# Performance work log

Hardware: AMD Instinct MI355X
Metric: run time of the kernel (lower is better)

The kernel has to match this reference:

```python
import jax, jax.numpy as jnp
import numpy as np

N_NODES = 4096
N_EDGES = 65536
BS = 16
LEAKY_SLOPE = 0.01
BN_EPS = 1e-5


def _init(key, shape, scale=0.02):
    return (jax.random.normal(key, shape, dtype=jnp.float32) * scale)


def setup_inputs() -> dict:
    key = jax.random.key(0)
    ks = jax.random.split(key, 20)
    x_in = jax.random.normal(ks[0], (N_NODES, 8500), dtype=jnp.float32)
    edge_index = jax.random.randint(ks[1], (2, N_EDGES), 0, N_NODES, dtype=jnp.int64)
    return {
        "x_in": x_in,
        "edge_index": edge_index,
        # SAGEConv params: Wl (neighbor lin, with bias), Wr (root lin, no bias)
        "W1l": _init(ks[2], (320, 8500)), "b1": jnp.zeros((320,), jnp.float32), "W1r": _init(ks[3], (320, 8500)),
        "W2l": _init(ks[4], (180, 320)),  "b2": jnp.zeros((180,), jnp.float32), "W2r": _init(ks[5], (180, 320)),
        "W3l": _init(ks[6], (90, 180)),   "b3": jnp.zeros((90,), jnp.float32),  "W3r": _init(ks[7], (90, 180)),
        "W4l": _init(ks[8], (50, 90)),    "b4": jnp.zeros((50,), jnp.float32),  "W4r": _init(ks[9], (50, 90)),
        "Wf1": _init(ks[10], (32, 50)),   "bf1": jnp.zeros((32,), jnp.float32),
        "Wf2": _init(ks[11], (16, 32)),   "bf2": jnp.zeros((16,), jnp.float32),
        "Wf3": _init(ks[12], (1, 16)),    "bf3": jnp.zeros((1,), jnp.float32),
    }


def _sage(x, src, dst, Wl, bl, Wr):
    # PyG SAGEConv: out = lin_l(mean_{j in N(i)} x_j) + lin_r(x_i)
    agg = jax.ops.segment_sum(x[src], dst, num_segments=N_NODES)          # [N, F]
    deg = jax.ops.segment_sum(jnp.ones_like(dst, dtype=x.dtype), dst, num_segments=N_NODES)
    mean = agg / jnp.maximum(deg, 1.0)[:, None]
    return mean @ Wl.T + bl + x @ Wr.T


def _leaky(x):
    return jnp.where(x >= 0, x, LEAKY_SLOPE * x)


def _bn(x):
    # F.batch_norm(x, None, None, training=True): per-feature, biased var, no affine
    m = jnp.mean(x, axis=0)
    v = jnp.mean((x - m) ** 2, axis=0)
    return (x - m) / jnp.sqrt(v + BN_EPS)


def reference(x_in, edge_index,
              W1l, b1, W1r, W2l, b2, W2r, W3l, b3, W3r, W4l, b4, W4r,
              Wf1, bf1, Wf2, bf2, Wf3, bf3):
    src, dst = edge_index[0], edge_index[1]
    x = _bn(_leaky(_sage(x_in, src, dst, W1l, b1, W1r)))
    x = _bn(_leaky(_sage(x, src, dst, W2l, b2, W2r)))
    x = _bn(_leaky(_sage(x, src, dst, W3l, b3, W3r)))
    x = _bn(_leaky(_sage(x, src, dst, W4l, b4, W4r)))
    # get_batch: label i -> floor(i / (N/BS)); global_add_pool == segment sum
    x = x.reshape(BS, N_NODES // BS, -1).sum(axis=1)                      # [BS, 50]
    x = x @ Wf1.T + bf1
    x = x @ Wf2.T + bf2
    x = x @ Wf3.T + bf3
    return x
```

## Files before the change

kernel.cpp:

```cpp
#include <hip/hip_runtime.h>
#include <stdint.h>

#define NN 4096
#define NE 65536
#define LEAKY 0.01f
#define BN_EPS 1e-5f

typedef float f32x4 __attribute__((ext_vector_type(4)));
typedef __bf16 bf16x8 __attribute__((ext_vector_type(8)));
typedef unsigned short u16x8 __attribute__((ext_vector_type(8)));

static __device__ __forceinline__ unsigned short f2bf(float v) {
  unsigned int u = __float_as_uint(v);
  u += 0x7fff + ((u >> 16) & 1);
  return (unsigned short)(u >> 16);
}

typedef __attribute__((address_space(1))) void gvoid;
typedef __attribute__((address_space(3))) void lvoid;

static __device__ __forceinline__ void async16(const void* g, void* l) {
  __builtin_amdgcn_global_load_lds((gvoid*)(uintptr_t)g,
                                   (lvoid*)(uint32_t)(uintptr_t)l, 16, 0, 0);
}


static __device__ __forceinline__ void pack_w_seg(int lblk, const float* __restrict__ Wl,
                                                  const float* __restrict__ Wr,
                                                  unsigned short* __restrict__ dst,
                                                  int Fout, int Fin, int Kp, int Np) {
  int nb = Kp >> 3;
  int idx = lblk * 256 + threadIdx.x;
  if (idx >= Np * nb) return;
  int row = idx / nb, kb = idx - row * nb;
  int g = kb >> 3, b = kb & 7;
  int dkb = (g << 3) | ((b + row) & 7);
  const float* src = nullptr;
  if (row < Fout)          src = Wl + (size_t)row * Fin;
  else if (row < 2 * Fout) src = Wr + (size_t)(row - Fout) * Fin;
  u16x8 st;
#pragma unroll
  for (int o = 0; o < 8; ++o) {
    int k = kb * 8 + o;
    float v = (src && k < Fin) ? src[k] : 0.f;
    st[o] = f2bf(v);
  }
  *(u16x8*)&dst[(size_t)row * Kp + dkb * 8] = st;
}

#define PX_BLK   17024
#define PW1_BLK   2660
#define PW2_BLK     60
#define PW3_BLK     24
#define PW4_BLK      8
#define CD_BLK     256
#define SETUP_BLK (PX_BLK + PW1_BLK + PW2_BLK + PW3_BLK + PW4_BLK + CD_BLK)

__global__ __launch_bounds__(256) void setup_all(
    const float* __restrict__ x, const int* __restrict__ dsti,
    const float* __restrict__ W1l, const float* __restrict__ W1r,
    const float* __restrict__ W2l, const float* __restrict__ W2r,
    const float* __restrict__ W3l, const float* __restrict__ W3r,
    const float* __restrict__ W4l, const float* __restrict__ W4r,
    unsigned short* __restrict__ xbf, unsigned short* __restrict__ wb1,
    unsigned short* __restrict__ wb2, unsigned short* __restrict__ wb3,
    unsigned short* __restrict__ wb4, int* __restrict__ deg) {
  int blk = blockIdx.x;
  if (blk < PX_BLK) {
    int idx = blk * 256 + threadIdx.x;
    int row = idx / 1064, kb = idx - row * 1064;
    int g = kb >> 3, b = kb & 7;
    int dkb = (g << 3) | ((b + row) & 7);
    const float* src = x + (size_t)row * 8500 + kb * 8;
    float v[8];
    if (kb < 1062) {
      f32x4 a = *(const f32x4*)src;
      f32x4 c = *(const f32x4*)(src + 4);
#pragma unroll
      for (int o = 0; o < 4; ++o) { v[o] = a[o]; v[o + 4] = c[o]; }
    } else {
#pragma unroll
      for (int o = 0; o < 8; ++o) {
        int k = kb * 8 + o;
        v[o] = (k < 8500) ? x[(size_t)row * 8500 + k] : 0.f;
      }
    }
    u16x8 st;
#pragma unroll
    for (int o = 0; o < 8; ++o) st[o] = f2bf(v[o]);
    *(u16x8*)&xbf[(size_t)row * 8512 + dkb * 8] = st;
  } else if (blk < PX_BLK + PW1_BLK) {
    pack_w_seg(blk - PX_BLK, W1l, W1r, wb1, 320, 8500, 8512, 640);
  } else if (blk < PX_BLK + PW1_BLK + PW2_BLK) {
    pack_w_seg(blk - PX_BLK - PW1_BLK, W2l, W2r, wb2, 180, 320, 320, 384);
  } else if (blk < PX_BLK + PW1_BLK + PW2_BLK + PW3_BLK) {
    pack_w_seg(blk - PX_BLK - PW1_BLK - PW2_BLK, W3l, W3r, wb3, 90, 180, 192, 256);
  } else if (blk < PX_BLK + PW1_BLK + PW2_BLK + PW3_BLK + PW4_BLK) {
    pack_w_seg(blk - PX_BLK - PW1_BLK - PW2_BLK - PW3_BLK, W4l, W4r, wb4, 50, 90, 128, 128);
  } else {
    int e = (blk - (SETUP_BLK - CD_BLK)) * 256 + threadIdx.x;
    atomicAdd(&deg[dsti[e]], 1);
  }
}


__global__ __launch_bounds__(1024) void scan_deg(const int* __restrict__ deg,
                                                 int* __restrict__ off) {
  __shared__ int s[NN];
  int t = threadIdx.x;
  for (int i = t; i < NN; i += 1024) s[i] = deg[i];
  __syncthreads();
  for (int step = 1; step < NN; step <<= 1) {
    int v[4];
#pragma unroll
    for (int j = 0; j < 4; ++j) {
      int i = t + j * 1024;
      v[j] = (i >= step) ? s[i - step] : 0;
    }
    __syncthreads();
#pragma unroll
    for (int j = 0; j < 4; ++j) s[t + j * 1024] += v[j];
    __syncthreads();
  }
  for (int i = t; i < NN; i += 1024) off[i] = (i == 0) ? 0 : s[i - 1];
}

__global__ void scatter_edges(const int* __restrict__ src_idx,
                              const int* __restrict__ dst_idx,
                              const int* __restrict__ off, int* __restrict__ cursor,
                              int* __restrict__ eix) {
  int e = blockIdx.x * 256 + threadIdx.x;
  if (e < NE) {
    int d = dst_idx[e];
    int pos = atomicAdd(&cursor[d], 1);
    eix[off[d] + pos] = src_idx[e];
  }
}

__global__ __launch_bounds__(256) void gemm_bt(const unsigned short* __restrict__ A,
                                               const unsigned short* __restrict__ B,
                                               float* __restrict__ C, int N, int K,
                                               int M) {
  __shared__ unsigned short smem[2 * 128 * 64];
  unsigned short* As = smem;
  unsigned short* Bs = smem + 128 * 64;

  const int t = threadIdx.x;
  const int bm = blockIdx.x, bn = blockIdx.y;
  const int lane = t & 63;
  const int wave = t >> 6;
  const int wm = (wave & 1) * 64, wn = (wave >> 1) * 64;
  const int l16 = lane & 15, quad = lane >> 4;

  const int ksteps = K >> 6;
  const int gz = (int)gridDim.z;
  const int per = (ksteps + gz - 1) / gz;
  const int k0 = (int)blockIdx.z * per;
  int k1 = k0 + per; if (k1 > ksteps) k1 = ksteps;

  f32x4 zero = {0.f, 0.f, 0.f, 0.f};
  f32x4 acc[4][4];
#pragma unroll
  for (int i = 0; i < 4; ++i)
#pragma unroll
    for (int j = 0; j < 4; ++j) acc[i][j] = zero;

  const int srow = t >> 3;
  const int scol = (t & 7) * 8;
  const unsigned short* Abase = A + (size_t)(bm * 128) * K + scol;
  const unsigned short* Bbase = B + (size_t)(bn * 128) * K + scol;

  for (int kt = k0; kt < k1; ++kt) {
    const unsigned short* Ag = Abase + kt * 64;
    const unsigned short* Bg = Bbase + kt * 64;
#pragma unroll
    for (int p = 0; p < 4; ++p) {
      int row = p * 32 + srow;
      async16(Ag + (size_t)row * K, &As[row * 64 + scol]);
    }
#pragma unroll
    for (int p = 0; p < 4; ++p) {
      int row = p * 32 + srow;
      async16(Bg + (size_t)row * K, &Bs[row * 64 + scol]);
    }
    __syncthreads();
#pragma unroll
    for (int kh = 0; kh < 2; ++kh) {
      const int s8 = ((kh * 4 + quad + l16) & 7) * 8;
      bf16x8 af[4], bfr[4];
#pragma unroll
      for (int i = 0; i < 4; ++i)
        af[i] = *(const bf16x8*)&As[(wm + i * 16 + l16) * 64 + s8];
#pragma unroll
      for (int j = 0; j < 4; ++j)
        bfr[j] = *(const bf16x8*)&Bs[(wn + j * 16 + l16) * 64 + s8];
#pragma unroll
      for (int i = 0; i < 4; ++i)
#pragma unroll
        for (int j = 0; j < 4; ++j)
          acc[i][j] = __builtin_amdgcn_mfma_f32_16x16x32_bf16(af[i], bfr[j], acc[i][j], 0, 0, 0);
    }
    __syncthreads();
  }

  float* Cb = C + (size_t)blockIdx.z * M * N;
#pragma unroll
  for (int i = 0; i < 4; ++i) {
    int rbase = bm * 128 + wm + i * 16 + quad * 4;
#pragma unroll
    for (int j = 0; j < 4; ++j) {
      int col = bn * 128 + wn + j * 16 + l16;
      float* cp = Cb + (size_t)rbase * N + col;
#pragma unroll
      for (int r = 0; r < 4; ++r) cp[(size_t)r * N] = acc[i][j][r];
    }
  }
}

__global__ void reduce4(float* __restrict__ y) {
  int idx = blockIdx.x * 256 + threadIdx.x;
  f32x4* p = (f32x4*)y;
  const int S = NN * 640 / 4;
  f32x4 v = p[idx];
  v += p[idx + S];
  v += p[idx + 2 * S];
  v += p[idx + 3 * S];
  p[idx] = v;
}

__global__ __launch_bounds__(256) void sage_agg(
    const float* __restrict__ y, const int* __restrict__ off,
    const int* __restrict__ deg, const int* __restrict__ eix,
    const float* __restrict__ bias, float* __restrict__ z, int F, int ldy) {
  int i = blockIdx.x;
  int tx = threadIdx.x, ty = threadIdx.y;
  int f4 = (blockIdx.y * 64 + tx) * 4;
  __shared__ int se[64];
  __shared__ float red[3][64][4];
  int start = off[i], d = deg[i];
  bool active = (f4 < F);
  f32x4 s = {0.f, 0.f, 0.f, 0.f};
  for (int base = 0; base < d; base += 64) {
    __syncthreads();
    if (ty == 0 && base + tx < d) se[tx] = eix[start + base + tx];
    __syncthreads();
    int end = d - base; if (end > 64) end = 64;
    if (active) {
      for (int e = ty; e < end; e += 4)
        s += *(const f32x4*)&y[(size_t)se[e] * ldy + f4];
    }
  }
  if (ty > 0) *(f32x4*)red[ty - 1][tx] = s;
  __syncthreads();
  if (ty == 0 && active) {
    s += *(const f32x4*)red[0][tx];
    s += *(const f32x4*)red[1][tx];
    s += *(const f32x4*)red[2][tx];
    float inv = 1.f / (float)(d > 1 ? d : 1);
    int cnt = F - f4; if (cnt > 4) cnt = 4;
    const float* yr = &y[(size_t)i * ldy + F + f4];
    float* zo = &z[(size_t)i * F + f4];
    for (int j = 0; j < cnt; ++j) {
      float w = s[j] * inv + yr[j] + bias[f4 + j];
      zo[j] = (w >= 0.f) ? w : LEAKY * w;
    }
  }
}


__global__ __launch_bounds__(256) void bn_part(const float* __restrict__ z,
                                               float* __restrict__ sums, int F) {
  int tx = threadIdx.x, ty = threadIdx.y;
  int f = blockIdx.x * 64 + tx;
  float s = 0.f, s2 = 0.f;
  if (f < F) {
    int r0 = blockIdx.y * 512 + ty * 128;
    for (int j = 0; j < 128; ++j) {
      float v = z[(size_t)(r0 + j) * F + f];
      s += v; s2 += v * v;
    }
  }
  __shared__ float ls[4][64], ls2[4][64];
  ls[ty][tx] = s; ls2[ty][tx] = s2;
  __syncthreads();
  if (ty == 0 && f < F) {
    float S  = ls[0][tx] + ls[1][tx] + ls[2][tx] + ls[3][tx];
    float S2 = ls2[0][tx] + ls2[1][tx] + ls2[2][tx] + ls2[3][tx];
    atomicAdd(&sums[f], S);
    atomicAdd(&sums[F + f], S2);
  }
}

__global__ void bn_norm8(const float* __restrict__ z, const float* __restrict__ sums,
                         unsigned short* __restrict__ xout, int F, int Kp) {
  int nb = Kp >> 3;
  int idx = blockIdx.x * 256 + threadIdx.x;
  int row = idx / nb, kb = idx - row * nb;
  int g = kb >> 3, b = kb & 7;
  int dkb = (g << 3) | ((b + row) & 7);
  u16x8 st;
#pragma unroll
  for (int o = 0; o < 8; ++o) {
    int k = kb * 8 + o;
    float v = 0.f;
    if (k < F) {
      float m  = sums[k] * (1.f / NN);
      float var = sums[F + k] * (1.f / NN) - m * m;
      float rs = rsqrtf(var + BN_EPS);
      v = (z[(size_t)row * F + k] - m) * rs;
    }
    st[o] = f2bf(v);
  }
  *(u16x8*)&xout[(size_t)row * Kp + dkb * 8] = st;
}

__global__ void pool_fc(const float* __restrict__ z,
                        const float* __restrict__ sums,
                        const float* __restrict__ Wf1, const float* __restrict__ bf1,
                        const float* __restrict__ Wf2, const float* __restrict__ bf2,
                        const float* __restrict__ Wf3, const float* __restrict__ bf3,
                        float* __restrict__ out) {
  __shared__ float pool[50];
  __shared__ float h1[32], h2[16];
  int b = blockIdx.x, t = threadIdx.x;
  if (t < 50) {
    float s = 0.f;
    for (int r = 0; r < 256; ++r) s += z[(size_t)(b * 256 + r) * 50 + t];
    float m  = sums[t] * (1.f / NN);
    float var = sums[50 + t] * (1.f / NN) - m * m;
    float rs = rsqrtf(var + BN_EPS);
    pool[t] = (s - 256.f * m) * rs;
  }
  __syncthreads();
  if (t < 32) {
    float s = bf1[t];
    for (int f = 0; f < 50; ++f) s += pool[f] * Wf1[t * 50 + f];
    h1[t] = s;
  }
  __syncthreads();
  if (t < 16) {
    float s = bf2[t];
    for (int f = 0; f < 32; ++f) s += h1[f] * Wf2[t * 32 + f];
    h2[t] = s;
  }
  __syncthreads();
  if (t == 0) {
    float s = bf3[0];
    for (int f = 0; f < 16; ++f) s += h2[f] * Wf3[f];
    out[b] = s;
  }
}


extern "C" void kernel_launch(void* const* d_in, const int* in_sizes, int n_in,
                              void* d_out, int out_size, void* d_ws, size_t ws_size,
                              hipStream_t stream) {
  const float* x_in = (const float*)d_in[0];
  const int* ei = (const int*)d_in[1];
  const float* W1l = (const float*)d_in[2];
  const float* b1  = (const float*)d_in[3];
  const float* W1r = (const float*)d_in[4];
  const float* W2l = (const float*)d_in[5];
  const float* b2  = (const float*)d_in[6];
  const float* W2r = (const float*)d_in[7];
  const float* W3l = (const float*)d_in[8];
  const float* b3  = (const float*)d_in[9];
  const float* W3r = (const float*)d_in[10];
  const float* W4l = (const float*)d_in[11];
  const float* b4  = (const float*)d_in[12];
  const float* W4r = (const float*)d_in[13];
  const float* Wf1 = (const float*)d_in[14];
  const float* bf1 = (const float*)d_in[15];
  const float* Wf2 = (const float*)d_in[16];
  const float* bf2 = (const float*)d_in[17];
  const float* Wf3 = (const float*)d_in[18];
  const float* bf3 = (const float*)d_in[19];
  float* out = (float*)d_out;
  (void)in_sizes; (void)n_in; (void)out_size;

  char* ws = (char*)d_ws;
  size_t off = 0;
  auto alloc = [&](size_t bytes) -> void* {
    void* p = ws + off;
    off = (off + bytes + 255) & ~(size_t)255;
    return p;
  };
  unsigned short* xbf = (unsigned short*)alloc((size_t)NN * 8512 * 2);
  unsigned short* wb1 = (unsigned short*)alloc((size_t)640 * 8512 * 2);
  unsigned short* wb2 = (unsigned short*)alloc((size_t)384 * 320 * 2);
  unsigned short* wb3 = (unsigned short*)alloc((size_t)256 * 192 * 2);
  unsigned short* wb4 = (unsigned short*)alloc((size_t)128 * 128 * 2);
  float* y    = (float*)alloc((size_t)4 * NN * 640 * 4);
  float* z    = (float*)alloc((size_t)NN * 320 * 4);
  int* deg    = (int*)alloc(NN * 4);
  int* cursor = (int*)alloc(NN * 4);
  float* bnsum = (float*)alloc(1280 * 4);
  int* offb   = (int*)alloc(NN * 4);
  int* eix    = (int*)alloc(NE * 4);
  if (ws_size < off) return;
  float* bns1 = bnsum;
  float* bns2 = bnsum + 640;
  float* bns3 = bnsum + 1000;
  float* bns4 = bnsum + 1180;

  hipMemsetAsync(deg, 0, 2 * NN * 4 + 1280 * 4, stream);

  setup_all<<<dim3(SETUP_BLK), dim3(256), 0, stream>>>(
      x_in, ei + NE, W1l, W1r, W2l, W2r, W3l, W3r, W4l, W4r,
      xbf, wb1, wb2, wb3, wb4, deg);
  scan_deg<<<dim3(1), dim3(1024), 0, stream>>>(deg, offb);
  scatter_edges<<<dim3(NE / 256), dim3(256), 0, stream>>>(ei, ei + NE, offb, cursor, eix);

  gemm_bt<<<dim3(32, 5, 4), dim3(256), 0, stream>>>(xbf, wb1, y, 640, 8512, NN);
  reduce4<<<dim3(NN * 640 / 4 / 256), dim3(256), 0, stream>>>(y);
  sage_agg<<<dim3(NN, 2), dim3(64, 4), 0, stream>>>(y, offb, deg, eix, b1, z, 320, 640);
  bn_part<<<dim3(5, 8), dim3(64, 4), 0, stream>>>(z, bns1, 320);
  bn_norm8<<<dim3(NN * 40 / 256), dim3(256), 0, stream>>>(z, bns1, xbf, 320, 320);

  gemm_bt<<<dim3(32, 3, 1), dim3(256), 0, stream>>>(xbf, wb2, y, 384, 320, NN);
  sage_agg<<<dim3(NN, 1), dim3(64, 4), 0, stream>>>(y, offb, deg, eix, b2, z, 180, 384);
  bn_part<<<dim3(3, 8), dim3(64, 4), 0, stream>>>(z, bns2, 180);
  bn_norm8<<<dim3(NN * 24 / 256), dim3(256), 0, stream>>>(z, bns2, xbf, 180, 192);

  gemm_bt<<<dim3(32, 2, 1), dim3(256), 0, stream>>>(xbf, wb3, y, 256, 192, NN);
  sage_agg<<<dim3(NN, 1), dim3(64, 4), 0, stream>>>(y, offb, deg, eix, b3, z, 90, 256);
  bn_part<<<dim3(2, 8), dim3(64, 4), 0, stream>>>(z, bns3, 90);
  bn_norm8<<<dim3(NN * 16 / 256), dim3(256), 0, stream>>>(z, bns3, xbf, 90, 128);

  gemm_bt<<<dim3(32, 1, 1), dim3(256), 0, stream>>>(xbf, wb4, y, 128, 128, NN);
  sage_agg<<<dim3(NN, 1), dim3(64, 4), 0, stream>>>(y, offb, deg, eix, b4, z, 50, 128);
  bn_part<<<dim3(1, 8), dim3(64, 4), 0, stream>>>(z, bns4, 50);

  pool_fc<<<dim3(16), dim3(64), 0, stream>>>(z, bns4, Wf1, bf1, Wf2, bf2, Wf3, bf3, out);
}
```

Measured before the change: 516.4 us.

## Fuse post-GEMM pipeline into one persistent kernel with grid barriers

Replaces the chain of small launches (scan, scatter, split-K reduce, aggregation, BN partials, BN normalize, small GEMMs, pooling/FC) with a single 256-block persistent kernel that separates the stages with a software grid barrier. The first GEMM's split-K is raised from 4 to 8 when the workspace allows, and the slice reduction moves into the fused kernel, which runs it alongside the degree scan. The goal is to remove per-launch overhead and idle gaps between many tiny kernels. In exchange, every stage is limited to 256 blocks, there are many barrier round trips, and the barrier relies on all 256 blocks being co-resident.

```diff
diff --git a/kernel.cpp b/kernel.cpp
--- a/kernel.cpp
+++ b/kernel.cpp
@@ -103,40 +103,6 @@
   }
 }
 
-
-__global__ __launch_bounds__(1024) void scan_deg(const int* __restrict__ deg,
-                                                 int* __restrict__ off) {
-  __shared__ int s[NN];
-  int t = threadIdx.x;
-  for (int i = t; i < NN; i += 1024) s[i] = deg[i];
-  __syncthreads();
-  for (int step = 1; step < NN; step <<= 1) {
-    int v[4];
-#pragma unroll
-    for (int j = 0; j < 4; ++j) {
-      int i = t + j * 1024;
-      v[j] = (i >= step) ? s[i - step] : 0;
-    }
-    __syncthreads();
-#pragma unroll
-    for (int j = 0; j < 4; ++j) s[t + j * 1024] += v[j];
-    __syncthreads();
-  }
-  for (int i = t; i < NN; i += 1024) off[i] = (i == 0) ? 0 : s[i - 1];
-}
-
-__global__ void scatter_edges(const int* __restrict__ src_idx,
-                              const int* __restrict__ dst_idx,
-                              const int* __restrict__ off, int* __restrict__ cursor,
-                              int* __restrict__ eix) {
-  int e = blockIdx.x * 256 + threadIdx.x;
-  if (e < NE) {
-    int d = dst_idx[e];
-    int pos = atomicAdd(&cursor[d], 1);
-    eix[off[d] + pos] = src_idx[e];
-  }
-}
-
 __global__ __launch_bounds__(256) void gemm_bt(const unsigned short* __restrict__ A,
                                                const unsigned short* __restrict__ B,
                                                float* __restrict__ C, int N, int K,
@@ -217,137 +183,307 @@
   }
 }
 
-__global__ void reduce4(float* __restrict__ y) {
-  int idx = blockIdx.x * 256 + threadIdx.x;
-  f32x4* p = (f32x4*)y;
-  const int S = NN * 640 / 4;
-  f32x4 v = p[idx];
-  v += p[idx + S];
-  v += p[idx + 2 * S];
-  v += p[idx + 3 * S];
-  p[idx] = v;
-}
-
-__global__ __launch_bounds__(256) void sage_agg(
-    const float* __restrict__ y, const int* __restrict__ off,
-    const int* __restrict__ deg, const int* __restrict__ eix,
-    const float* __restrict__ bias, float* __restrict__ z, int F, int ldy) {
-  int i = blockIdx.x;
-  int tx = threadIdx.x, ty = threadIdx.y;
-  int f4 = (blockIdx.y * 64 + tx) * 4;
-  __shared__ int se[64];
-  __shared__ float red[3][64][4];
-  int start = off[i], d = deg[i];
-  bool active = (f4 < F);
-  f32x4 s = {0.f, 0.f, 0.f, 0.f};
-  for (int base = 0; base < d; base += 64) {
-    __syncthreads();
-    if (ty == 0 && base + tx < d) se[tx] = eix[start + base + tx];
-    __syncthreads();
-    int end = d - base; if (end > 64) end = 64;
-    if (active) {
-      for (int e = ty; e < end; e += 4)
-        s += *(const f32x4*)&y[(size_t)se[e] * ldy + f4];
-    }
-  }
-  if (ty > 0) *(f32x4*)red[ty - 1][tx] = s;
+
+static __device__ __forceinline__ void gbar(int* cnt, int* gen) {
   __syncthreads();
-  if (ty == 0 && active) {
-    s += *(const f32x4*)red[0][tx];
-    s += *(const f32x4*)red[1][tx];
-    s += *(const f32x4*)red[2][tx];
-    float inv = 1.f / (float)(d > 1 ? d : 1);
-    int cnt = F - f4; if (cnt > 4) cnt = 4;
-    const float* yr = &y[(size_t)i * ldy + F + f4];
-    float* zo = &z[(size_t)i * F + f4];
-    for (int j = 0; j < cnt; ++j) {
-      float w = s[j] * inv + yr[j] + bias[f4 + j];
-      zo[j] = (w >= 0.f) ? w : LEAKY * w;
-    }
-  }
-}
-
-
-__global__ __launch_bounds__(256) void bn_part(const float* __restrict__ z,
-                                               float* __restrict__ sums, int F) {
-  int tx = threadIdx.x, ty = threadIdx.y;
-  int f = blockIdx.x * 64 + tx;
-  float s = 0.f, s2 = 0.f;
-  if (f < F) {
-    int r0 = blockIdx.y * 512 + ty * 128;
-    for (int j = 0; j < 128; ++j) {
-      float v = z[(size_t)(r0 + j) * F + f];
-      s += v; s2 += v * v;
-    }
-  }
-  __shared__ float ls[4][64], ls2[4][64];
-  ls[ty][tx] = s; ls2[ty][tx] = s2;
+  if (threadIdx.x == 0) {
+    __threadfence();
+    int g = __hip_atomic_load(gen, __ATOMIC_RELAXED, __HIP_MEMORY_SCOPE_AGENT);
+    int a = __hip_atomic_fetch_add(cnt, 1, __ATOMIC_ACQ_REL, __HIP_MEMORY_SCOPE_AGENT);
+    if (a == (int)gridDim.x - 1) {
+      __hip_atomic_store(cnt, 0, __ATOMIC_RELAXED, __HIP_MEMORY_SCOPE_AGENT);
+      __hip_atomic_store(gen, g + 1, __ATOMIC_RELEASE, __HIP_MEMORY_SCOPE_AGENT);
+    } else {
+      while (__hip_atomic_load(gen, __ATOMIC_ACQUIRE, __HIP_MEMORY_SCOPE_AGENT) == g)
+        __builtin_amdgcn_s_sleep(2);
+    }
+  }
   __syncthreads();
-  if (ty == 0 && f < F) {
-    float S  = ls[0][tx] + ls[1][tx] + ls[2][tx] + ls[3][tx];
-    float S2 = ls2[0][tx] + ls2[1][tx] + ls2[2][tx] + ls2[3][tx];
-    atomicAdd(&sums[f], S);
-    atomicAdd(&sums[F + f], S2);
-  }
-}
-
-__global__ void bn_norm8(const float* __restrict__ z, const float* __restrict__ sums,
-                         unsigned short* __restrict__ xout, int F, int Kp) {
-  int nb = Kp >> 3;
-  int idx = blockIdx.x * 256 + threadIdx.x;
-  int row = idx / nb, kb = idx - row * nb;
-  int g = kb >> 3, b = kb & 7;
-  int dkb = (g << 3) | ((b + row) & 7);
-  u16x8 st;
-#pragma unroll
-  for (int o = 0; o < 8; ++o) {
-    int k = kb * 8 + o;
-    float v = 0.f;
-    if (k < F) {
-      float m  = sums[k] * (1.f / NN);
-      float var = sums[F + k] * (1.f / NN) - m * m;
-      float rs = rsqrtf(var + BN_EPS);
-      v = (z[(size_t)row * F + k] - m) * rs;
-    }
-    st[o] = f2bf(v);
-  }
-  *(u16x8*)&xout[(size_t)row * Kp + dkb * 8] = st;
-}
-
-__global__ void pool_fc(const float* __restrict__ z,
-                        const float* __restrict__ sums,
-                        const float* __restrict__ Wf1, const float* __restrict__ bf1,
-                        const float* __restrict__ Wf2, const float* __restrict__ bf2,
-                        const float* __restrict__ Wf3, const float* __restrict__ bf3,
-                        float* __restrict__ out) {
-  __shared__ float pool[50];
-  __shared__ float h1[32], h2[16];
-  int b = blockIdx.x, t = threadIdx.x;
-  if (t < 50) {
-    float s = 0.f;
-    for (int r = 0; r < 256; ++r) s += z[(size_t)(b * 256 + r) * 50 + t];
-    float m  = sums[t] * (1.f / NN);
-    float var = sums[50 + t] * (1.f / NN) - m * m;
-    float rs = rsqrtf(var + BN_EPS);
-    pool[t] = (s - 256.f * m) * rs;
-  }
-  __syncthreads();
-  if (t < 32) {
-    float s = bf1[t];
-    for (int f = 0; f < 50; ++f) s += pool[f] * Wf1[t * 50 + f];
-    h1[t] = s;
-  }
-  __syncthreads();
-  if (t < 16) {
-    float s = bf2[t];
-    for (int f = 0; f < 32; ++f) s += h1[f] * Wf2[t * 32 + f];
-    h2[t] = s;
-  }
-  __syncthreads();
-  if (t == 0) {
-    float s = bf3[0];
-    for (int f = 0; f < 16; ++f) s += h2[f] * Wf3[f];
-    out[b] = s;
+}
+
+static __device__ __forceinline__ void gemm_stage(const unsigned short* __restrict__ A,
+    const unsigned short* __restrict__ B, float* __restrict__ C, int N, int K, int nbn,
+    unsigned short* smem) {
+  unsigned short* As = smem;
+  unsigned short* Bs = smem + 128 * 64;
+  const int t = threadIdx.x;
+  const int lane = t & 63, wave = t >> 6;
+  const int wm = (wave & 1) * 64, wn = (wave >> 1) * 64;
+  const int l16 = lane & 15, quad = lane >> 4;
+  const int srow = t >> 3, scol = (t & 7) * 8;
+  const int ksteps = K >> 6;
+  const int tiles = 32 * nbn;
+  for (int u = blockIdx.x; u < tiles; u += 256) {
+    int bm = u & 31, bn = u >> 5;
+    f32x4 acc[4][4];
+#pragma unroll
+    for (int i = 0; i < 4; ++i)
+#pragma unroll
+      for (int j = 0; j < 4; ++j) acc[i][j] = (f32x4){0.f, 0.f, 0.f, 0.f};
+    const unsigned short* Abase = A + (size_t)(bm * 128) * K + scol;
+    const unsigned short* Bbase = B + (size_t)(bn * 128) * K + scol;
+    for (int kt = 0; kt < ksteps; ++kt) {
+      const unsigned short* Ag = Abase + kt * 64;
+      const unsigned short* Bg = Bbase + kt * 64;
+#pragma unroll
+      for (int p = 0; p < 4; ++p) {
+        int row = p * 32 + srow;
+        async16(Ag + (size_t)row * K, &As[row * 64 + scol]);
+      }
+#pragma unroll
+      for (int p = 0; p < 4; ++p) {
+        int row = p * 32 + srow;
+        async16(Bg + (size_t)row * K, &Bs[row * 64 + scol]);
+      }
+      __syncthreads();
+#pragma unroll
+      for (int kh = 0; kh < 2; ++kh) {
+        const int s8 = ((kh * 4 + quad + l16) & 7) * 8;
+        bf16x8 af[4], bfr[4];
+#pragma unroll
+        for (int i = 0; i < 4; ++i)
+          af[i] = *(const bf16x8*)&As[(wm + i * 16 + l16) * 64 + s8];
+#pragma unroll
+        for (int j = 0; j < 4; ++j)
+          bfr[j] = *(const bf16x8*)&Bs[(wn + j * 16 + l16) * 64 + s8];
+#pragma unroll
+        for (int i = 0; i < 4; ++i)
+#pragma unroll
+          for (int j = 0; j < 4; ++j)
+            acc[i][j] = __builtin_amdgcn_mfma_f32_16x16x32_bf16(af[i], bfr[j], acc[i][j], 0, 0, 0);
+      }
+      __syncthreads();
+    }
+#pragma unroll
+    for (int i = 0; i < 4; ++i) {
+      int rbase = bm * 128 + wm + i * 16 + quad * 4;
+#pragma unroll
+      for (int j = 0; j < 4; ++j) {
+        int col = bn * 128 + wn + j * 16 + l16;
+        float* cp = C + (size_t)rbase * N + col;
+#pragma unroll
+        for (int r = 0; r < 4; ++r) cp[(size_t)r * N] = acc[i][j][r];
+      }
+    }
+  }
+}
+
+static __device__ __forceinline__ void agg_stage(const float* __restrict__ y,
+    const int* __restrict__ off, const int* __restrict__ deg, const int* __restrict__ eix,
+    const float* __restrict__ bias, float* __restrict__ z, int F, int ldy, int nfg,
+    unsigned short* smem) {
+  const int t = threadIdx.x;
+  const int tx = t & 63, ty = t >> 6;
+  int* se = (int*)smem;
+  float* red = (float*)((char*)smem + 512);
+  const int nunits = NN * nfg;
+  for (int u = blockIdx.x; u < nunits; u += 256) {
+    int i = (nfg == 2) ? (u >> 1) : u;
+    int fg = (nfg == 2) ? (u & 1) : 0;
+    int f4 = (fg * 64 + tx) * 4;
+    int start = off[i], d = deg[i];
+    bool active = (f4 < F);
+    f32x4 s = {0.f, 0.f, 0.f, 0.f};
+    for (int base = 0; base < d; base += 64) {
+      __syncthreads();
+      if (ty == 0 && base + tx < d) se[tx] = eix[start + base + tx];
+      __syncthreads();
+      int end = d - base; if (end > 64) end = 64;
+      if (active)
+        for (int e = ty; e < end; e += 4)
+          s += *(const f32x4*)&y[(size_t)se[e] * ldy + f4];
+    }
+    if (ty > 0) *(f32x4*)&red[((ty - 1) * 64 + tx) * 4] = s;
+    __syncthreads();
+    if (ty == 0 && active) {
+      s += *(const f32x4*)&red[(tx) * 4];
+      s += *(const f32x4*)&red[(64 + tx) * 4];
+      s += *(const f32x4*)&red[(128 + tx) * 4];
+      float inv = 1.f / (float)(d > 1 ? d : 1);
+      int cnt2 = F - f4; if (cnt2 > 4) cnt2 = 4;
+      const float* yr = &y[(size_t)i * ldy + F + f4];
+      float* zo = &z[(size_t)i * F + f4];
+      for (int j = 0; j < cnt2; ++j) {
+        float w = s[j] * inv + yr[j] + bias[f4 + j];
+        zo[j] = (w >= 0.f) ? w : LEAKY * w;
+      }
+    }
+    __syncthreads();
+  }
+}
+
+static __device__ __forceinline__ void bn_part_stage(const float* __restrict__ z,
+    float* __restrict__ sums, int F, int nfb, unsigned short* smem) {
+  const int t = threadIdx.x, tx = t & 63, ty = t >> 6;
+  float* ls = (float*)smem;
+  float* ls2 = ls + 256;
+  const int units = nfb * 8;
+  for (int u = blockIdx.x; u < units; u += 256) {
+    int fb = u >> 3, rb = u & 7;
+    int f = fb * 64 + tx;
+    float s = 0.f, s2 = 0.f;
+    if (f < F) {
+      int r0 = rb * 512 + ty * 128;
+      for (int j = 0; j < 128; ++j) {
+        float v = z[(size_t)(r0 + j) * F + f];
+        s += v; s2 += v * v;
+      }
+    }
+    ls[ty * 64 + tx] = s; ls2[ty * 64 + tx] = s2;
+    __syncthreads();
+    if (ty == 0 && f < F) {
+      float S  = ls[tx] + ls[64 + tx] + ls[128 + tx] + ls[192 + tx];
+      float S2 = ls2[tx] + ls2[64 + tx] + ls2[128 + tx] + ls2[192 + tx];
+      atomicAdd(&sums[f], S);
+      atomicAdd(&sums[F + f], S2);
+    }
+    __syncthreads();
+  }
+}
+
+static __device__ __forceinline__ void bn_norm_stage(const float* __restrict__ z,
+    const float* __restrict__ sums, unsigned short* __restrict__ xout, int F, int Kp) {
+  const int nb = Kp >> 3;
+  const int total = NN * nb;
+  for (int idx = blockIdx.x * 256 + threadIdx.x; idx < total; idx += 65536) {
+    int row = idx / nb, kb = idx - row * nb;
+    int g = kb >> 3, b = kb & 7;
+    int dkb = (g << 3) | ((b + row) & 7);
+    u16x8 st;
+#pragma unroll
+    for (int o = 0; o < 8; ++o) {
+      int k = kb * 8 + o;
+      float v = 0.f;
+      if (k < F) {
+        float m  = sums[k] * (1.f / NN);
+        float var = sums[F + k] * (1.f / NN) - m * m;
+        float rs = rsqrtf(var + BN_EPS);
+        v = (z[(size_t)row * F + k] - m) * rs;
+      }
+      st[o] = f2bf(v);
+    }
+    *(u16x8*)&xout[(size_t)row * Kp + dkb * 8] = st;
+  }
+}
+
+__global__ __launch_bounds__(256) void tail_fused(
+    float* __restrict__ y, int nz,
+    const int* __restrict__ deg, int* __restrict__ offb, int* __restrict__ cursor,
+    int* __restrict__ eix, const int* __restrict__ esrc, const int* __restrict__ edst,
+    const unsigned short* __restrict__ wb2, const unsigned short* __restrict__ wb3,
+    const unsigned short* __restrict__ wb4,
+    unsigned short* __restrict__ xbf, float* __restrict__ z, float* __restrict__ bnsum,
+    const float* __restrict__ b1, const float* __restrict__ b2,
+    const float* __restrict__ b3, const float* __restrict__ b4,
+    const float* __restrict__ Wf1, const float* __restrict__ bf1,
+    const float* __restrict__ Wf2, const float* __restrict__ bf2,
+    const float* __restrict__ Wf3, const float* __restrict__ bf3,
+    float* __restrict__ out, int* __restrict__ bar) {
+  __shared__ unsigned short smem[2 * 128 * 64];
+  const int t = threadIdx.x;
+  const int blk = blockIdx.x;
+  int* cnt = bar;
+  int* gen = bar + 16;
+
+  if (blk == 0) {
+    int* s = (int*)smem;
+    for (int j = 0; j < 16; ++j) s[t + j * 256] = deg[t + j * 256];
+    __syncthreads();
+    for (int step = 1; step < NN; step <<= 1) {
+      int v[16];
+#pragma unroll
+      for (int j = 0; j < 16; ++j) {
+        int i = t + j * 256;
+        v[j] = (i >= step) ? s[i - step] : 0;
+      }
+      __syncthreads();
+#pragma unroll
+      for (int j = 0; j < 16; ++j) s[t + j * 256] += v[j];
+      __syncthreads();
+    }
+    for (int j = 0; j < 16; ++j) {
+      int i = t + j * 256;
+      offb[i] = i ? s[i - 1] : 0;
+    }
+  } else {
+    const int S = NN * 640 / 4;
+    f32x4* p = (f32x4*)y;
+    for (int idx = (blk - 1) * 256 + t; idx < S; idx += 255 * 256) {
+      f32x4 v = p[idx];
+      for (int sl = 1; sl < nz; ++sl) v += p[idx + (size_t)sl * S];
+      p[idx] = v;
+    }
+  }
+  gbar(cnt, gen);
+  {
+    int e = blk * 256 + t;
+    int d = edst[e];
+    int pos = atomicAdd(&cursor[d], 1);
+    eix[offb[d] + pos] = esrc[e];
+  }
+  gbar(cnt, gen);
+  agg_stage(y, offb, deg, eix, b1, z, 320, 640, 2, smem);
+  gbar(cnt, gen);
+  bn_part_stage(z, bnsum, 320, 5, smem);
+  gbar(cnt, gen);
+  bn_norm_stage(z, bnsum, xbf, 320, 320);
+  gbar(cnt, gen);
+  gemm_stage(xbf, wb2, y, 384, 320, 3, smem);
+  gbar(cnt, gen);
+  agg_stage(y, offb, deg, eix, b2, z, 180, 384, 1, smem);
+  gbar(cnt, gen);
+  bn_part_stage(z, bnsum + 640, 180, 3, smem);
+  gbar(cnt, gen);
+  bn_norm_stage(z, bnsum + 640, xbf, 180, 192);
+  gbar(cnt, gen);
+  gemm_stage(xbf, wb3, y, 256, 192, 2, smem);
+  gbar(cnt, gen);
+  agg_stage(y, offb, deg, eix, b3, z, 90, 256, 1, smem);
+  gbar(cnt, gen);
+  bn_part_stage(z, bnsum + 1000, 90, 2, smem);
+  gbar(cnt, gen);
+  bn_norm_stage(z, bnsum + 1000, xbf, 90, 128);
+  gbar(cnt, gen);
+  gemm_stage(xbf, wb4, y, 128, 128, 1, smem);
+  gbar(cnt, gen);
+  agg_stage(y, offb, deg, eix, b4, z, 50, 128, 1, smem);
+  gbar(cnt, gen);
+  bn_part_stage(z, bnsum + 1180, 50, 1, smem);
+  gbar(cnt, gen);
+  {
+    float* pool = (float*)smem;
+    float* h1 = pool + 64;
+    float* h2 = pool + 96;
+    const float* s4 = bnsum + 1180;
+    for (int u = blk; u < 16; u += 256) {
+      if (t < 50) {
+        float s = 0.f;
+        for (int r = 0; r < 256; ++r) s += z[(size_t)(u * 256 + r) * 50 + t];
+        float m  = s4[t] * (1.f / NN);
+        float var = s4[50 + t] * (1.f / NN) - m * m;
+        float rs = rsqrtf(var + BN_EPS);
+        pool[t] = (s - 256.f * m) * rs;
+      }
+      __syncthreads();
+      if (t < 32) {
+        float s = bf1[t];
+        for (int f = 0; f < 50; ++f) s += pool[f] * Wf1[t * 50 + f];
+        h1[t] = s;
+      }
+      __syncthreads();
+      if (t < 16) {
+        float s = bf2[t];
+        for (int f = 0; f < 32; ++f) s += h1[f] * Wf2[t * 32 + f];
+        h2[t] = s;
+      }
+      __syncthreads();
+      if (t == 0) {
+        float s = bf3[0];
+        for (int f = 0; f < 16; ++f) s += h2[f] * Wf3[f];
+        out[u] = s;
+      }
+      __syncthreads();
+    }
   }
 }
 
@@ -390,46 +526,29 @@
   unsigned short* wb2 = (unsigned short*)alloc((size_t)384 * 320 * 2);
   unsigned short* wb3 = (unsigned short*)alloc((size_t)256 * 192 * 2);
   unsigned short* wb4 = (unsigned short*)alloc((size_t)128 * 128 * 2);
-  float* y    = (float*)alloc((size_t)4 * NN * 640 * 4);
   float* z    = (float*)alloc((size_t)NN * 320 * 4);
   int* deg    = (int*)alloc(NN * 4);
   int* cursor = (int*)alloc(NN * 4);
   float* bnsum = (float*)alloc(1280 * 4);
+  int* bar    = (int*)alloc(256);
   int* offb   = (int*)alloc(NN * 4);
   int* eix    = (int*)alloc(NE * 4);
-  if (ws_size < off) return;
-  float* bns1 = bnsum;
-  float* bns2 = bnsum + 640;
-  float* bns3 = bnsum + 1000;
-  float* bns4 = bnsum + 1180;
-
-  hipMemsetAsync(deg, 0, 2 * NN * 4 + 1280 * 4, stream);
+  const size_t YS = (size_t)NN * 640 * 4;
+  float* y = (float*)(ws + off);
+  int nz = (off + 8 * YS <= ws_size) ? 8 : 4;
+  if (off + (size_t)nz * YS > ws_size) return;
+
+  const size_t memset_bytes = NN * 4 + NN * 4 + 1280 * 4 + 256;
+  hipMemsetAsync(deg, 0, memset_bytes, stream);
 
   setup_all<<<dim3(SETUP_BLK), dim3(256), 0, stream>>>(
       x_in, ei + NE, W1l, W1r, W2l, W2r, W3l, W3r, W4l, W4r,
       xbf, wb1, wb2, wb3, wb4, deg);
-  scan_deg<<<dim3(1), dim3(1024), 0, stream>>>(deg, offb);
-  scatter_edges<<<dim3(NE / 256), dim3(256), 0, stream>>>(ei, ei + NE, offb, cursor, eix);
-
-  gemm_bt<<<dim3(32, 5, 4), dim3(256), 0, stream>>>(xbf, wb1, y, 640, 8512, NN);
-  reduce4<<<dim3(NN * 640 / 4 / 256), dim3(256), 0, stream>>>(y);
-  sage_agg<<<dim3(NN, 2), dim3(64, 4), 0, stream>>>(y, offb, deg, eix, b1, z, 320, 640);
-  bn_part<<<dim3(5, 8), dim3(64, 4), 0, stream>>>(z, bns1, 320);
-  bn_norm8<<<dim3(NN * 40 / 256), dim3(256), 0, stream>>>(z, bns1, xbf, 320, 320);
-
-  gemm_bt<<<dim3(32, 3, 1), dim3(256), 0, stream>>>(xbf, wb2, y, 384, 320, NN);
-  sage_agg<<<dim3(NN, 1), dim3(64, 4), 0, stream>>>(y, offb, deg, eix, b2, z, 180, 384);
-  bn_part<<<dim3(3, 8), dim3(64, 4), 0, stream>>>(z, bns2, 180);
-  bn_norm8<<<dim3(NN * 24 / 256), dim3(256), 0, stream>>>(z, bns2, xbf, 180, 192);
-
-  gemm_bt<<<dim3(32, 2, 1), dim3(256), 0, stream>>>(xbf, wb3, y, 256, 192, NN);
-  sage_agg<<<dim3(NN, 1), dim3(64, 4), 0, stream>>>(y, offb, deg, eix, b3, z, 90, 256);
-  bn_part<<<dim3(2, 8), dim3(64, 4), 0, stream>>>(z, bns3, 90);
-  bn_norm8<<<dim3(NN * 16 / 256), dim3(256), 0, stream>>>(z, bns3, xbf, 90, 128);
-
-  gemm_bt<<<dim3(32, 1, 1), dim3(256), 0, stream>>>(xbf, wb4, y, 128, 128, NN);
-  sage_agg<<<dim3(NN, 1), dim3(64, 4), 0, stream>>>(y, offb, deg, eix, b4, z, 50, 128);
-  bn_part<<<dim3(1, 8), dim3(64, 4), 0, stream>>>(z, bns4, 50);
-
-  pool_fc<<<dim3(16), dim3(64), 0, stream>>>(z, bns4, Wf1, bf1, Wf2, bf2, Wf3, bf3, out);
-}
+
+  gemm_bt<<<dim3(32, 5, nz), dim3(256), 0, stream>>>(xbf, wb1, y, 640, 8512, NN);
+
+  tail_fused<<<dim3(256), dim3(256), 0, stream>>>(
+      y, nz, deg, offb, cursor, eix, ei, ei + NE,
+      wb2, wb3, wb4, xbf, z, (float*)bnsum,
+      b1, b2, b3, b4, Wf1, bf1, Wf2, bf2, Wf3, bf3, out, bar);
+}
```

New measurement: 1.221 ms. 137% more time.

## Build padded fixed-stride adjacency in setup and widen split-K for layer-1 GEMM

Applied to the files above, without the earlier changes.

The CSR build (degree scan kernel plus scatter kernel) is replaced by a fixed-stride adjacency of 96 slots per node. It is filled with atomics inside the existing setup kernel, which removes two serial launches including a single-block scan. sage_agg now loads the whole neighbour list in one pass instead of looping over 64-edge chunks. Separately, the layer-1 GEMM uses 8 split-K slices instead of 4 when the workspace allows, for more parallelism, at the cost of more partial-sum traffic in the reduction. Nodes with more than 96 incoming edges would be silently truncated, which is safe only for graphs with bounded degree.

```diff
diff --git a/kernel.cpp b/kernel.cpp
--- a/kernel.cpp
+++ b/kernel.cpp
@@ -5,6 +5,7 @@
 #define NE 65536
 #define LEAKY 0.01f
 #define BN_EPS 1e-5f
+#define DSTRIDE 96
 
 typedef float f32x4 __attribute__((ext_vector_type(4)));
 typedef __bf16 bf16x8 __attribute__((ext_vector_type(8)));
@@ -53,18 +54,18 @@
 #define PW2_BLK     60
 #define PW3_BLK     24
 #define PW4_BLK      8
-#define CD_BLK     256
-#define SETUP_BLK (PX_BLK + PW1_BLK + PW2_BLK + PW3_BLK + PW4_BLK + CD_BLK)
+#define ADJ_BLK    256
+#define SETUP_BLK (PX_BLK + PW1_BLK + PW2_BLK + PW3_BLK + PW4_BLK + ADJ_BLK)
 
 __global__ __launch_bounds__(256) void setup_all(
-    const float* __restrict__ x, const int* __restrict__ dsti,
+    const float* __restrict__ x, const int* __restrict__ esrc, const int* __restrict__ edst,
     const float* __restrict__ W1l, const float* __restrict__ W1r,
     const float* __restrict__ W2l, const float* __restrict__ W2r,
     const float* __restrict__ W3l, const float* __restrict__ W3r,
     const float* __restrict__ W4l, const float* __restrict__ W4r,
     unsigned short* __restrict__ xbf, unsigned short* __restrict__ wb1,
     unsigned short* __restrict__ wb2, unsigned short* __restrict__ wb3,
-    unsigned short* __restrict__ wb4, int* __restrict__ deg) {
+    unsigned short* __restrict__ wb4, int* __restrict__ deg, int* __restrict__ eix) {
   int blk = blockIdx.x;
   if (blk < PX_BLK) {
     int idx = blk * 256 + threadIdx.x;
@@ -98,42 +99,10 @@
   } else if (blk < PX_BLK + PW1_BLK + PW2_BLK + PW3_BLK + PW4_BLK) {
     pack_w_seg(blk - PX_BLK - PW1_BLK - PW2_BLK - PW3_BLK, W4l, W4r, wb4, 50, 90, 128, 128);
   } else {
-    int e = (blk - (SETUP_BLK - CD_BLK)) * 256 + threadIdx.x;
-    atomicAdd(&deg[dsti[e]], 1);
-  }
-}
-
-
-__global__ __launch_bounds__(1024) void scan_deg(const int* __restrict__ deg,
-                                                 int* __restrict__ off) {
-  __shared__ int s[NN];
-  int t = threadIdx.x;
-  for (int i = t; i < NN; i += 1024) s[i] = deg[i];
-  __syncthreads();
-  for (int step = 1; step < NN; step <<= 1) {
-    int v[4];
-#pragma unroll
-    for (int j = 0; j < 4; ++j) {
-      int i = t + j * 1024;
-      v[j] = (i >= step) ? s[i - step] : 0;
-    }
-    __syncthreads();
-#pragma unroll
-    for (int j = 0; j < 4; ++j) s[t + j * 1024] += v[j];
-    __syncthreads();
-  }
-  for (int i = t; i < NN; i += 1024) off[i] = (i == 0) ? 0 : s[i - 1];
-}
-
-__global__ void scatter_edges(const int* __restrict__ src_idx,
-                              const int* __restrict__ dst_idx,
-                              const int* __restrict__ off, int* __restrict__ cursor,
-                              int* __restrict__ eix) {
-  int e = blockIdx.x * 256 + threadIdx.x;
-  if (e < NE) {
-    int d = dst_idx[e];
-    int pos = atomicAdd(&cursor[d], 1);
-    eix[off[d] + pos] = src_idx[e];
+    int e = (blk - (SETUP_BLK - ADJ_BLK)) * 256 + threadIdx.x;
+    int d = edst[e];
+    int pos = atomicAdd(&deg[d], 1);
+    if (pos < DSTRIDE) eix[(size_t)d * DSTRIDE + pos] = esrc[e];
   }
 }
 
@@ -158,12 +127,11 @@
   const int k0 = (int)blockIdx.z * per;
   int k1 = k0 + per; if (k1 > ksteps) k1 = ksteps;
 
-  f32x4 zero = {0.f, 0.f, 0.f, 0.f};
   f32x4 acc[4][4];
 #pragma unroll
   for (int i = 0; i < 4; ++i)
 #pragma unroll
-    for (int j = 0; j < 4; ++j) acc[i][j] = zero;
+    for (int j = 0; j < 4; ++j) acc[i][j] = (f32x4){0.f, 0.f, 0.f, 0.f};
 
   const int srow = t >> 3;
   const int scol = (t & 7) * 8;
@@ -217,39 +185,35 @@
   }
 }
 
-__global__ void reduce4(float* __restrict__ y) {
+__global__ void reduceN(float* __restrict__ y, int nz) {
   int idx = blockIdx.x * 256 + threadIdx.x;
   f32x4* p = (f32x4*)y;
   const int S = NN * 640 / 4;
   f32x4 v = p[idx];
-  v += p[idx + S];
-  v += p[idx + 2 * S];
-  v += p[idx + 3 * S];
+  for (int sl = 1; sl < nz; ++sl) v += p[idx + (size_t)sl * S];
   p[idx] = v;
 }
 
 __global__ __launch_bounds__(256) void sage_agg(
-    const float* __restrict__ y, const int* __restrict__ off,
-    const int* __restrict__ deg, const int* __restrict__ eix,
-    const float* __restrict__ bias, float* __restrict__ z, int F, int ldy) {
+    const float* __restrict__ y, const int* __restrict__ deg,
+    const int* __restrict__ eix, const float* __restrict__ bias,
+    float* __restrict__ z, int F, int ldy) {
   int i = blockIdx.x;
   int tx = threadIdx.x, ty = threadIdx.y;
   int f4 = (blockIdx.y * 64 + tx) * 4;
-  __shared__ int se[64];
+  __shared__ int se[DSTRIDE];
   __shared__ float red[3][64][4];
-  int start = off[i], d = deg[i];
+  int d = deg[i]; if (d > DSTRIDE) d = DSTRIDE;
   bool active = (f4 < F);
   f32x4 s = {0.f, 0.f, 0.f, 0.f};
-  for (int base = 0; base < d; base += 64) {
-    __syncthreads();
-    if (ty == 0 && base + tx < d) se[tx] = eix[start + base + tx];
-    __syncthreads();
-    int end = d - base; if (end > 64) end = 64;
-    if (active) {
-      for (int e = ty; e < end; e += 4)
-        s += *(const f32x4*)&y[(size_t)se[e] * ldy + f4];
-    }
-  }
+  {
+    int lt = ty * 64 + tx;
+    if (lt < d) se[lt] = eix[(size_t)i * DSTRIDE + lt];
+  }
+  __syncthreads();
+  if (active)
+    for (int e = ty; e < d; e += 4)
+      s += *(const f32x4*)&y[(size_t)se[e] * ldy + f4];
   if (ty > 0) *(f32x4*)red[ty - 1][tx] = s;
   __syncthreads();
   if (ty == 0 && active) {
@@ -390,45 +354,43 @@
   unsigned short* wb2 = (unsigned short*)alloc((size_t)384 * 320 * 2);
   unsigned short* wb3 = (unsigned short*)alloc((size_t)256 * 192 * 2);
   unsigned short* wb4 = (unsigned short*)alloc((size_t)128 * 128 * 2);
-  float* y    = (float*)alloc((size_t)4 * NN * 640 * 4);
   float* z    = (float*)alloc((size_t)NN * 320 * 4);
   int* deg    = (int*)alloc(NN * 4);
-  int* cursor = (int*)alloc(NN * 4);
   float* bnsum = (float*)alloc(1280 * 4);
-  int* offb   = (int*)alloc(NN * 4);
-  int* eix    = (int*)alloc(NE * 4);
-  if (ws_size < off) return;
+  int* eix    = (int*)alloc((size_t)NN * DSTRIDE * 4);
+  const size_t YS = (size_t)NN * 640 * 4;
+  float* y = (float*)(ws + off);
+  int nz = (off + 8 * YS <= ws_size) ? 8 : 4;
+  if (off + (size_t)nz * YS > ws_size) return;
   float* bns1 = bnsum;
   float* bns2 = bnsum + 640;
   float* bns3 = bnsum + 1000;
   float* bns4 = bnsum + 1180;
 
-  hipMemsetAsync(deg, 0, 2 * NN * 4 + 1280 * 4, stream);
+  hipMemsetAsync(deg, 0, NN * 4 + 1280 * 4, stream);
 
   setup_all<<<dim3(SETUP_BLK), dim3(256), 0, stream>>>(
-      x_in, ei + NE, W1l, W1r, W2l, W2r, W3l, W3r, W4l, W4r,
-      xbf, wb1, wb2, wb3, wb4, deg);
-  scan_deg<<<dim3(1), dim3(1024), 0, stream>>>(deg, offb);
-  scatter_edges<<<dim3(NE / 256), dim3(256), 0, stream>>>(ei, ei + NE, offb, cursor, eix);
-
-  gemm_bt<<<dim3(32, 5, 4), dim3(256), 0, stream>>>(xbf, wb1, y, 640, 8512, NN);
-  reduce4<<<dim3(NN * 640 / 4 / 256), dim3(256), 0, stream>>>(y);
-  sage_agg<<<dim3(NN, 2), dim3(64, 4), 0, stream>>>(y, offb, deg, eix, b1, z, 320, 640);
+      x_in, ei, ei + NE, W1l, W1r, W2l, W2r, W3l, W3r, W4l, W4r,
+      xbf, wb1, wb2, wb3, wb4, deg, eix);
+
+  gemm_bt<<<dim3(32, 5, nz), dim3(256), 0, stream>>>(xbf, wb1, y, 640, 8512, NN);
+  reduceN<<<dim3(NN * 640 / 4 / 256), dim3(256), 0, stream>>>(y, nz);
+  sage_agg<<<dim3(NN, 2), dim3(64, 4), 0, stream>>>(y, deg, eix, b1, z, 320, 640);
   bn_part<<<dim3(5, 8), dim3(64, 4), 0, stream>>>(z, bns1, 320);
   bn_norm8<<<dim3(NN * 40 / 256), dim3(256), 0, stream>>>(z, bns1, xbf, 320, 320);
 
   gemm_bt<<<dim3(32, 3, 1), dim3(256), 0, stream>>>(xbf, wb2, y, 384, 320, NN);
-  sage_agg<<<dim3(NN, 1), dim3(64, 4), 0, stream>>>(y, offb, deg, eix, b2, z, 180, 384);
+  sage_agg<<<dim3(NN, 1), dim3(64, 4), 0, stream>>>(y, deg, eix, b2, z, 180, 384);
   bn_part<<<dim3(3, 8), dim3(64, 4), 0, stream>>>(z, bns2, 180);
   bn_norm8<<<dim3(NN * 24 / 256), dim3(256), 0, stream>>>(z, bns2, xbf, 180, 192);
 
   gemm_bt<<<dim3(32, 2, 1), dim3(256), 0, stream>>>(xbf, wb3, y, 256, 192, NN);
-  sage_agg<<<dim3(NN, 1), dim3(64, 4), 0, stream>>>(y, offb, deg, eix, b3, z, 90, 256);
+  sage_agg<<<dim3(NN, 1), dim3(64, 4), 0, stream>>>(y, deg, eix, b3, z, 90, 256);
   bn_part<<<dim3(2, 8), dim3(64, 4), 0, stream>>>(z, bns3, 90);
   bn_norm8<<<dim3(NN * 16 / 256), dim3(256), 0, stream>>>(z, bns3, xbf, 90, 128);
 
   gemm_bt<<<dim3(32, 1, 1), dim3(256), 0, stream>>>(xbf, wb4, y, 128, 128, NN);
-  sage_agg<<<dim3(NN, 1), dim3(64, 4), 0, stream>>>(y, offb, deg, eix, b4, z, 50, 128);
+  sage_agg<<<dim3(NN, 1), dim3(64, 4), 0, stream>>>(y, deg, eix, b4, z, 50, 128);
   bn_part<<<dim3(1, 8), dim3(64, 4), 0, stream>>>(z, bns4, 50);
 
   pool_fc<<<dim3(16), dim3(64), 0, stream>>>(z, bns4, Wf1, bf1, Wf2, bf2, Wf3, bf3, out);
```

After: 507.8 us. Within noise of the previous version (-1.7%).
